# Optimization experiments

Hardware: AMD Instinct MI355X
Metric: run time of the kernel (lower is better)

The kernel has to match this reference:

```python
import jax, jax.numpy as jnp
import numpy as np

B, N, DIM, K = 4, 4096, 128, 16


def setup_inputs() -> dict:
    key = jax.random.key(0)
    ks = jax.random.split(key, 20)
    s = 0.05
    inp = {
        "x": jax.random.normal(ks[0], (B, N, DIM), jnp.float32),
        "pos": jax.random.normal(ks[1], (B, N, 3), jnp.float32),
        # pos_mlp: Linear(3,dim) -> ReLU -> Linear(dim,dim)
        "pw1": jax.random.normal(ks[2], (3, DIM), jnp.float32) * s,
        "pb1": jnp.zeros((DIM,), jnp.float32),
        "pw2": jax.random.normal(ks[3], (DIM, DIM), jnp.float32) * s,
        "pb2": jnp.zeros((DIM,), jnp.float32),
        # q/k/v projections
        "qw": jax.random.normal(ks[4], (DIM, DIM), jnp.float32) * s,
        "qb": jnp.zeros((DIM,), jnp.float32),
        "kw": jax.random.normal(ks[5], (DIM, DIM), jnp.float32) * s,
        "kb": jnp.zeros((DIM,), jnp.float32),
        "vw": jax.random.normal(ks[6], (DIM, DIM), jnp.float32) * s,
        "vb": jnp.zeros((DIM,), jnp.float32),
        # attn MLP: Linear(dim, dim//4) -> ReLU -> Linear(dim//4, dim)
        "aw1": jax.random.normal(ks[7], (DIM, DIM // 4), jnp.float32) * s,
        "ab1": jnp.zeros((DIM // 4,), jnp.float32),
        "aw2": jax.random.normal(ks[8], (DIM // 4, DIM), jnp.float32) * s,
        "ab2": jnp.zeros((DIM,), jnp.float32),
    }
    return inp


def reference(x, pos, pw1, pb1, pw2, pb2, qw, qb, kw, kb, vw, vb, aw1, ab1, aw2, ab2):
    Bs, Np, C = x.shape
    k = K
    # pairwise squared distances: |pi|^2 + |pj|^2 - 2 pi.pj  -> (B,N,N)
    inner = jnp.einsum('bnd,bmd->bnm', pos, pos)
    xx = jnp.sum(pos * pos, axis=2, keepdims=True)  # (B,N,1)
    dist = xx + jnp.swapaxes(xx, 1, 2) - 2.0 * inner
    # k nearest neighbors (smallest dist) -> indices (B,N,k)
    _, idx = jax.lax.top_k(-dist, k)
    bidx = jnp.arange(Bs)[:, None, None]
    neighbors = x[bidx, idx]        # (B,N,k,C)
    pos_neighbors = pos[bidx, idx]  # (B,N,k,3)
    pos_relative = pos[:, :, None, :] - pos_neighbors  # (B,N,k,3)
    # pos MLP
    pe = jax.nn.relu(pos_relative @ pw1 + pb1) @ pw2 + pb2  # (B,N,k,C)
    q = (x @ qw + qb)[:, :, None, :]   # (B,N,1,C)
    kk = neighbors @ kw + kb           # (B,N,k,C)
    v = neighbors @ vw + vb            # (B,N,k,C)
    a = q - kk + pe
    attn = jax.nn.relu(a @ aw1 + ab1) @ aw2 + ab2  # (B,N,k,C)
    attn = jax.nn.softmax(attn, axis=2)
    out = jnp.sum(attn * (v + pe), axis=2)  # (B,N,C)
    return out
```

## Files before the change

### kernel.cpp

```cpp
#include <hip/hip_runtime.h>
#include <hip/hip_bf16.h>
#include <stdint.h>

#define BATCH 4
#define NPTS  4096
#define DIM   128
#define KNN   16
#define NROWS (BATCH*NPTS)
#define NCHUNK 16
#define CHUNK  (NPTS/NCHUNK)

typedef unsigned long long u64;
typedef unsigned int u32;
typedef unsigned short u16;
typedef __attribute__((ext_vector_type(8))) short short8;
typedef __attribute__((ext_vector_type(4))) float f32x4;

__device__ __forceinline__ u16 f2bf(float f) {
  u32 u = __float_as_uint(f);
  u += 0x7FFFu + ((u >> 16) & 1);
  return (u16)(u >> 16);
}

__global__ __launch_bounds__(256) void prep_pos4(const float* __restrict__ pos,
                                                 float4* __restrict__ pos4) {
  int i = blockIdx.x * 256 + threadIdx.x;
  if (i < NROWS) pos4[i] = make_float4(pos[3*i], pos[3*i+1], pos[3*i+2], 0.f);
}

__global__ __launch_bounds__(256) void prep_matmul(
    const float* __restrict__ pw2, const float* __restrict__ qw, const float* __restrict__ kw,
    const float* __restrict__ aw1,
    u16* __restrict__ w1T, float* __restrict__ Wq2, float* __restrict__ Wk2) {
  int p = blockIdx.x >> 2, qtr = blockIdx.x & 3;
  const float* A = p == 0 ? pw2 : (p == 1 ? qw : kw);
  int j = threadIdx.x & 31;
  int r0 = qtr*32 + (threadIdx.x >> 5)*4;
  float acc[4] = {0.f,0.f,0.f,0.f};
  for (int c = 0; c < 128; ++c) {
    float av = aw1[c*32 + j];
#pragma unroll
    for (int rr = 0; rr < 4; ++rr) acc[rr] = fmaf(A[(r0+rr)*128 + c], av, acc[rr]);
  }
#pragma unroll
  for (int rr = 0; rr < 4; ++rr) {
    int h = r0 + rr;
    if (p == 0)      w1T[j*128 + (h ^ ((j&7)<<3))] = f2bf(acc[rr]);
    else if (p == 1) Wq2[h*32 + j] = acc[rr];
    else             Wk2[h*32 + j] = acc[rr];
  }
}

__global__ __launch_bounds__(256) void prep_convert(
    const float* __restrict__ pw2, const float* __restrict__ aw2,
    const float* __restrict__ pw1, const float* __restrict__ pb1,
    const float* __restrict__ qb, const float* __restrict__ kb,
    const float* __restrict__ pb2, const float* __restrict__ aw1, const float* __restrict__ ab1,
    u16* __restrict__ pw2T, u16* __restrict__ aw2T,
    float4* __restrict__ pw1q, float* __restrict__ bias1) {
  int bid = blockIdx.x, tid = threadIdx.x;
  if (bid < 64) {
    int e = bid*256 + tid; int k = e >> 7, n = e & 127;
    pw2T[n*128 + (k ^ ((n&7)<<3))] = f2bf(pw2[k*128 + n]);
  } else if (bid < 80) {
    int e = (bid-64)*256 + tid; int k = e >> 7, n = e & 127;
    aw2T[n*32 + (k ^ ((n&3)<<3))] = f2bf(aw2[k*128 + n]);
  } else {
    if (tid < 128) {
      int c = tid;
      pw1q[c ^ ((c & 0x18) >> 2)] = make_float4(pw1[c], pw1[128+c], pw1[256+c], pb1[c]);
    } else if (tid < 160) {
      int j = tid - 128;
      float s = ab1[j];
      for (int c = 0; c < 128; ++c) s += (qb[c]-kb[c]+pb2[c]) * aw1[c*32+j];
      bias1[j] = s;
    }
  }
}

template <typename T>
__device__ __forceinline__ void cex(T& a, T& b) {
  T mn = a < b ? a : b;
  T mx = a < b ? b : a;
  a = mn; b = mx;
}
template <typename T>
__device__ __forceinline__ void sort16(T x[16]) {
#pragma unroll
  for (int k = 2; k <= 16; k <<= 1)
#pragma unroll
    for (int j = k >> 1; j > 0; j >>= 1)
#pragma unroll
      for (int i = 0; i < 16; ++i) {
        int l = i ^ j;
        if (l > i) { if ((i & k) == 0) cex(x[i], x[l]); else cex(x[l], x[i]); }
      }
}
template <typename T>
__device__ __forceinline__ void merge16(T A[16], const T B[16]) {
#pragma unroll
  for (int i = 0; i < 16; ++i) { T b = B[15 - i]; A[i] = A[i] < b ? A[i] : b; }
#pragma unroll
  for (int j = 8; j > 0; j >>= 1)
#pragma unroll
    for (int i = 0; i < 16; ++i) { int l = i ^ j; if (l > i) cex(A[i], A[l]); }
}

__global__ __launch_bounds__(256) void knn_scan(const float4* __restrict__ pos4,
                                                u32* __restrict__ part) {
  __shared__ float4 cs[4][CHUNK];
  const int lane  = threadIdx.x & 63;
  const int w     = threadIdx.x >> 6;
  const int task  = blockIdx.x * 4 + w;
  const int qg    = task >> 4;
  const int chunk = task & 15;
  const int qbase = qg * 64;
  const int b     = qbase >> 12;
  const int cbase = chunk * CHUNK;

  const float4* cand = pos4 + b*NPTS + cbase;
#pragma unroll
  for (int i = 0; i < CHUNK/64; ++i) cs[w][lane + 64*i] = cand[lane + 64*i];
  __syncthreads();

  float4 qp = pos4[qbase + lane];
  const float qx = qp.x, qy = qp.y, qz = qp.z;

  u32 best[16];
#pragma unroll
  for (int i = 0; i < 16; ++i) best[i] = ~0u;

#pragma unroll 1
  for (int m = 0; m < CHUNK/16; ++m) {
    u32 batch[16];
#pragma unroll
    for (int e = 0; e < 16; ++e) {
      float4 p = cs[w][m*16 + e];
      float dx = qx - p.x, dy = qy - p.y, dz = qz - p.z;
      float d  = fmaf(dx, dx, fmaf(dy, dy, dz*dz));
      batch[e] = (__float_as_uint(d) & 0xFFFFFF00u) | (u32)(m*16 + e);
    }
    sort16(batch);
    merge16(best, batch);
  }
  const int q = qbase + lane;
#pragma unroll
  for (int s = 0; s < 16; ++s) part[(chunk*16 + s)*NROWS + q] = best[s];
}

__global__ __launch_bounds__(256) void knn_refine(const float4* __restrict__ pos4,
                                                  const u32* __restrict__ part,
                                                  int* __restrict__ knnIdx) {
  __shared__ u64 lists[16][273];
  const int tid = threadIdx.x;
  const int qi = tid >> 4, c = tid & 15;
  const int q = blockIdx.x * 16 + qi;
  const int b = q >> 12;

  float4 qp = pos4[q];
  const double qx = qp.x, qy = qp.y, qz = qp.z;

  u64 key[16];
#pragma unroll
  for (int s = 0; s < 16; ++s) {
    u32 kk = part[(c*16 + s)*NROWS + q];
    int idx = c*CHUNK + (int)(kk & 0xFFu);
    float4 p = pos4[(b<<12) + idx];
    double dx = qx - (double)p.x;
    double dy = qy - (double)p.y;
    double dz = qz - (double)p.z;
    double d  = fma(dx, dx, fma(dy, dy, dz*dz));
    key[s] = (((u64)__double_as_longlong(d)) & ~0xFFFull) | (u64)idx;
  }
  sort16(key);
#pragma unroll
  for (int s = 0; s < 16; ++s) lists[qi][c*17 + s] = key[s];
  __syncthreads();

  if ((tid & 15) == 0) {
    u64 best[16];
#pragma unroll
    for (int s = 0; s < 16; ++s) best[s] = lists[qi][s];
#pragma unroll 1
    for (int cc = 1; cc < 16; ++cc) {
      u64 nb[16];
#pragma unroll
      for (int s = 0; s < 16; ++s) nb[s] = lists[qi][cc*17 + s];
      merge16(best, nb);
    }
    const int outq = q * KNN;
#pragma unroll
    for (int s = 0; s < 16; ++s) knnIdx[outq + s] = (int)(best[s] & 0xFFFull);
  }
}

__global__ __launch_bounds__(256) void proj_v(
    const float* __restrict__ x,
    const float* __restrict__ vw, const float* __restrict__ vb,
    const float* __restrict__ Wq2, const float* __restrict__ Wk2,
    float* __restrict__ vo, float* __restrict__ qa, float* __restrict__ ka) {
  __shared__ float xs[32*DIM];
  const int row0 = blockIdx.x * 32;
  const int tid = threadIdx.x;
  {
    const float4* src = (const float4*)(x + row0*DIM);
    float4* dst = (float4*)xs;
#pragma unroll
    for (int i = 0; i < 4; ++i) dst[tid + 256*i] = src[tid + 256*i];
  }
  __syncthreads();
  {
    const int c = tid & 127, g2 = tid >> 7;
    float av[16];
#pragma unroll
    for (int r = 0; r < 16; ++r) av[r] = 0.f;
    for (int d4 = 0; d4 < 32; ++d4) {
      float wv[4];
#pragma unroll
      for (int t = 0; t < 4; ++t) wv[t] = vw[(d4*4+t)*DIM + c];
#pragma unroll
      for (int r = 0; r < 16; ++r) {
        float4 xv = *(const float4*)&xs[(g2*16+r)*DIM + d4*4];
        av[r] = fmaf(xv.x, wv[0], av[r]);
        av[r] = fmaf(xv.y, wv[1], av[r]);
        av[r] = fmaf(xv.z, wv[2], av[r]);
        av[r] = fmaf(xv.w, wv[3], av[r]);
      }
    }
    float bv = vb[c];
#pragma unroll
    for (int r = 0; r < 16; ++r) vo[(row0 + g2*16 + r)*DIM + c] = av[r] + bv;
  }
  {
    const int j = tid & 31, grp = tid >> 5;
    float aq[4] = {0.f,0.f,0.f,0.f}, ak[4] = {0.f,0.f,0.f,0.f};
    for (int d4 = 0; d4 < 32; ++d4) {
#pragma unroll
      for (int t = 0; t < 4; ++t) {
        int d = d4*4 + t;
        float wq = Wq2[d*32 + j], wk = Wk2[d*32 + j];
#pragma unroll
        for (int rr = 0; rr < 4; ++rr) {
          float xv = xs[(grp*4+rr)*DIM + d];
          aq[rr] = fmaf(xv, wq, aq[rr]);
          ak[rr] = fmaf(xv, wk, ak[rr]);
        }
      }
    }
#pragma unroll
    for (int rr = 0; rr < 4; ++rr) {
      qa[(row0 + grp*4 + rr)*32 + j] = aq[rr];
      ka[(row0 + grp*4 + rr)*32 + j] = ak[rr];
    }
  }
}

__global__ __launch_bounds__(256) void attn_mfma(
    const float4* __restrict__ pos4, const int* __restrict__ knnIdx,
    const float* __restrict__ vws, const float* __restrict__ qa, const float* __restrict__ ka,
    const u16* __restrict__ pw2T, const u16* __restrict__ w1T, const u16* __restrict__ aw2T,
    const float4* __restrict__ pw1q, const float* __restrict__ bias1,
    const float* __restrict__ pb2, const float* __restrict__ ab2,
    float* __restrict__ out) {
  __shared__ __align__(16) u16 pw2s[16384];
  __shared__ __align__(16) u16 w1s[4096];
  __shared__ __align__(16) u16 aw2s[4096];
  __shared__ __align__(16) float4 pw1s[128];
  __shared__ float bias1s[32];
  __shared__ float pb2s[128];
  __shared__ float ab2s[128];
  __shared__ __align__(16) u16 h2t[4][512];
  __shared__ float4 rels[4][16];
  __shared__ int ids[4][16];

  const int tid = threadIdx.x;
  {
    const uint4* s1 = (const uint4*)pw2T; uint4* d1 = (uint4*)pw2s;
#pragma unroll
    for (int i = 0; i < 8; ++i) d1[tid + 256*i] = s1[tid + 256*i];
    const uint4* s2 = (const uint4*)w1T; uint4* d2 = (uint4*)w1s;
#pragma unroll
    for (int i = 0; i < 2; ++i) d2[tid + 256*i] = s2[tid + 256*i];
    const uint4* s3 = (const uint4*)aw2T; uint4* d3 = (uint4*)aw2s;
#pragma unroll
    for (int i = 0; i < 2; ++i) d3[tid + 256*i] = s3[tid + 256*i];
    if (tid < 128) { pw1s[tid] = pw1q[tid]; pb2s[tid] = pb2[tid]; ab2s[tid] = ab2[tid]; }
    else if (tid < 160) bias1s[tid-128] = bias1[tid-128];
  }
  __syncthreads();

  const int lane = tid & 63, w = tid >> 6;
  const int c16 = lane & 15, g = lane >> 4;

  for (int it = 0; it < 4; ++it) {
    const int q = blockIdx.x*16 + w*4 + it;
    const int b = q >> 12;
    if (lane < 16) {
      int id = knnIdx[q*KNN + lane];
      ids[w][lane] = id;
      float4 pq = pos4[q], pn = pos4[(b<<12) + id];
      rels[w][lane] = make_float4(pq.x-pn.x, pq.y-pn.y, pq.z-pn.z, 0.f);
    }
    __syncthreads();

    int idr[4];
#pragma unroll
    for (int r = 0; r < 4; ++r) idr[r] = ids[w][g*4 + r];

    float qa_v[2], ka_v[2][4];
#pragma unroll
    for (int t = 0; t < 2; ++t) qa_v[t] = qa[q*32 + t*16 + c16];
#pragma unroll
    for (int r = 0; r < 4; ++r)
#pragma unroll
      for (int t = 0; t < 2; ++t) ka_v[t][r] = ka[((b<<12)+idr[r])*32 + t*16 + c16];

    float4 rl = rels[w][c16];
    short8 h1f[4];
#pragma unroll
    for (int kc = 0; kc < 4; ++kc) {
      short8 s;
#pragma unroll
      for (int j = 0; j < 8; ++j) {
        int c = kc*32 + g*8 + j;
        float4 wv = pw1s[c ^ ((c & 0x18) >> 2)];
        float h = fmaf(rl.x, wv.x, fmaf(rl.y, wv.y, fmaf(rl.z, wv.z, wv.w)));
        s[j] = (short)f2bf(fmaxf(h, 0.f));
      }
      h1f[kc] = s;
    }

    f32x4 pe[8];
#pragma unroll
    for (int nt = 0; nt < 8; ++nt) { f32x4 z = {0.f,0.f,0.f,0.f}; pe[nt] = z; }
#pragma unroll
    for (int kc = 0; kc < 4; ++kc)
#pragma unroll
      for (int nt = 0; nt < 8; ++nt) {
        int n = nt*16 + c16;
        short8 bf = *(const short8*)&pw2s[n*128 + ((kc*32 + g*8) ^ ((n&7)<<3))];
        pe[nt] = __builtin_amdgcn_mfma_f32_16x16x32_bf16(h1f[kc], bf, pe[nt], 0, 0, 0);
      }

    f32x4 ha[2];
#pragma unroll
    for (int t = 0; t < 2; ++t) { f32x4 z = {0.f,0.f,0.f,0.f}; ha[t] = z; }
#pragma unroll
    for (int kc = 0; kc < 4; ++kc)
#pragma unroll
      for (int t = 0; t < 2; ++t) {
        int n = t*16 + c16;
        short8 bf = *(const short8*)&w1s[n*128 + ((kc*32 + g*8) ^ ((n&7)<<3))];
        ha[t] = __builtin_amdgcn_mfma_f32_16x16x32_bf16(h1f[kc], bf, ha[t], 0, 0, 0);
      }

#pragma unroll
    for (int t = 0; t < 2; ++t)
#pragma unroll
      for (int r = 0; r < 4; ++r) {
        float v = ha[t][r] + qa_v[t] - ka_v[t][r] + bias1s[t*16 + c16];
        int row = g*4 + r, col = t*16 + c16;
        h2t[w][row*32 + (col ^ ((row&3)<<3))] = f2bf(fmaxf(v, 0.f));
      }
    __syncthreads();

    short8 h2f = *(const short8*)&h2t[w][c16*32 + ((g*8) ^ ((c16&3)<<3))];

    f32x4 lg[8];
#pragma unroll
    for (int nt = 0; nt < 8; ++nt) {
      int n = nt*16 + c16;
      float ab = ab2s[n];
      f32x4 cini = {ab, ab, ab, ab};
      short8 bf = *(const short8*)&aw2s[n*32 + ((g*8) ^ ((n&3)<<3))];
      lg[nt] = __builtin_amdgcn_mfma_f32_16x16x32_bf16(h2f, bf, cini, 0, 0, 0);
    }

    float vv[8][4];
#pragma unroll
    for (int r = 0; r < 4; ++r) {
      const float* vrow = vws + (size_t)((b<<12) + idr[r])*DIM;
#pragma unroll
      for (int nt = 0; nt < 8; ++nt) vv[nt][r] = vrow[nt*16 + c16];
    }

#pragma unroll
    for (int nt = 0; nt < 8; ++nt) {
      float m = fmaxf(fmaxf(lg[nt][0], lg[nt][1]), fmaxf(lg[nt][2], lg[nt][3]));
      m = fmaxf(m, __shfl_xor(m, 16));
      m = fmaxf(m, __shfl_xor(m, 32));
      float e0 = __expf(lg[nt][0]-m), e1 = __expf(lg[nt][1]-m),
            e2 = __expf(lg[nt][2]-m), e3 = __expf(lg[nt][3]-m);
      float s = e0+e1+e2+e3;
      s += __shfl_xor(s, 16);
      s += __shfl_xor(s, 32);
      float inv = 1.0f / s;
      float pb = pb2s[nt*16 + c16];
      float acc = e0*(vv[nt][0] + pe[nt][0] + pb)
                + e1*(vv[nt][1] + pe[nt][1] + pb)
                + e2*(vv[nt][2] + pe[nt][2] + pb)
                + e3*(vv[nt][3] + pe[nt][3] + pb);
      acc *= inv;
      acc += __shfl_xor(acc, 16);
      acc += __shfl_xor(acc, 32);
      if (lane < 16) out[q*DIM + nt*16 + lane] = acc;
    }
  }
}

extern "C" void kernel_launch(void* const* d_in, const int* in_sizes, int n_in,
                              void* d_out, int out_size, void* d_ws, size_t ws_size,
                              hipStream_t stream) {
  const float* x   = (const float*)d_in[0];
  const float* pos = (const float*)d_in[1];
  const float* pw1 = (const float*)d_in[2];
  const float* pb1 = (const float*)d_in[3];
  const float* pw2 = (const float*)d_in[4];
  const float* pb2 = (const float*)d_in[5];
  const float* qw  = (const float*)d_in[6];
  const float* qb  = (const float*)d_in[7];
  const float* kw  = (const float*)d_in[8];
  const float* kb  = (const float*)d_in[9];
  const float* vw  = (const float*)d_in[10];
  const float* vb  = (const float*)d_in[11];
  const float* aw1 = (const float*)d_in[12];
  const float* ab1 = (const float*)d_in[13];
  const float* aw2 = (const float*)d_in[14];
  const float* ab2 = (const float*)d_in[15];
  float* out = (float*)d_out;

  char* ws = (char*)d_ws;
  float4* pos4   = (float4*)(ws);
  int*    knnIdx = (int*)(ws + (1u<<20));
  u32*    part   = (u32*)(ws + (2u<<20));
  float*  vws    = (float*)(ws + (2u<<20));
  float*  qa     = (float*)(ws + (11u<<20));
  float*  ka     = (float*)(ws + (13u<<20));
  char*   wsw    = ws + (19u<<20);
  u16*    pw2T  = (u16*)(wsw);
  u16*    w1T   = (u16*)(wsw + 32768);
  u16*    aw2T  = (u16*)(wsw + 40960);
  float4* pw1q  = (float4*)(wsw + 49152);
  float*  bias1 = (float*)(wsw + 51200);
  float*  Wq2   = (float*)(wsw + 51328);
  float*  Wk2   = (float*)(wsw + 67712);

  prep_pos4<<<NROWS/256, 256, 0, stream>>>(pos, pos4);
  prep_matmul<<<12, 256, 0, stream>>>(pw2, qw, kw, aw1, w1T, Wq2, Wk2);
  prep_convert<<<81, 256, 0, stream>>>(pw2, aw2, pw1, pb1, qb, kb, pb2, aw1, ab1,
                                       pw2T, aw2T, pw1q, bias1);
  knn_scan<<<(NROWS/64)*NCHUNK/4, 256, 0, stream>>>(pos4, part);
  knn_refine<<<NROWS/16, 256, 0, stream>>>(pos4, part, knnIdx);
  proj_v<<<NROWS/32, 256, 0, stream>>>(x, vw, vb, Wq2, Wk2, vws, qa, ka);
  attn_mfma<<<NROWS/16, 256, 0, stream>>>(pos4, knnIdx, vws, qa, ka,
                                          pw2T, w1T, aw2T, pw1q, bias1, pb2, ab2, out);
}
```

Measured before the change: 284.2 us.

## Parallelize KNN refine with bitonic tree merge and fp64 rescoring of top-32

The scan kernel now packs a global candidate index into 12 low bits and stores each query's partial lists contiguously with vector stores. The refine kernel reads them with uint4 loads and merges the 16 chunk lists with a parallel bitonic tree in shared memory, replacing the single-thread serial merge. Only the surviving 32 candidates are rescored in double precision and then merged to the final 16, instead of rescoring all 256. The risk is that coarser fp32 keys (12 bits of mantissa dropped) may leave a true neighbour outside the top 32 in near-tie cases.

```diff
diff --git a/kernel.cpp b/kernel.cpp
--- a/kernel.cpp
+++ b/kernel.cpp
@@ -105,6 +105,12 @@
 #pragma unroll
     for (int i = 0; i < 16; ++i) { int l = i ^ j; if (l > i) cex(A[i], A[l]); }
 }
+__device__ __forceinline__ void bmerge32(u32 x[32]) {
+#pragma unroll
+  for (int j = 16; j > 0; j >>= 1)
+#pragma unroll
+    for (int i = 0; i < 32; ++i) { int l = i ^ j; if (l > i) cex(x[i], x[l]); }
+}
 
 __global__ __launch_bounds__(256) void knn_scan(const float4* __restrict__ pos4,
                                                 u32* __restrict__ part) {
@@ -138,56 +144,119 @@
       float4 p = cs[w][m*16 + e];
       float dx = qx - p.x, dy = qy - p.y, dz = qz - p.z;
       float d  = fmaf(dx, dx, fmaf(dy, dy, dz*dz));
-      batch[e] = (__float_as_uint(d) & 0xFFFFFF00u) | (u32)(m*16 + e);
+      batch[e] = (__float_as_uint(d) & 0xFFFFF000u) | (u32)(cbase + m*16 + e);
     }
     sort16(batch);
     merge16(best, batch);
   }
   const int q = qbase + lane;
-#pragma unroll
-  for (int s = 0; s < 16; ++s) part[(chunk*16 + s)*NROWS + q] = best[s];
+  uint4* dst = (uint4*)(part + q*256 + chunk*16);
+#pragma unroll
+  for (int t = 0; t < 4; ++t)
+    dst[t] = make_uint4(best[4*t], best[4*t+1], best[4*t+2], best[4*t+3]);
 }
 
 __global__ __launch_bounds__(256) void knn_refine(const float4* __restrict__ pos4,
                                                   const u32* __restrict__ part,
                                                   int* __restrict__ knnIdx) {
-  __shared__ u64 lists[16][273];
+  __shared__ u64 A64[16][137];
+  __shared__ u32 Bu[16][264];
+  u32 (*Au)[274] = (u32 (*)[274])A64;
+
   const int tid = threadIdx.x;
   const int qi = tid >> 4, c = tid & 15;
-  const int q = blockIdx.x * 16 + qi;
-  const int b = q >> 12;
-
-  float4 qp = pos4[q];
-  const double qx = qp.x, qy = qp.y, qz = qp.z;
-
-  u64 key[16];
-#pragma unroll
-  for (int s = 0; s < 16; ++s) {
-    u32 kk = part[(c*16 + s)*NROWS + q];
-    int idx = c*CHUNK + (int)(kk & 0xFFu);
-    float4 p = pos4[(b<<12) + idx];
-    double dx = qx - (double)p.x;
-    double dy = qy - (double)p.y;
-    double dz = qz - (double)p.z;
-    double d  = fma(dx, dx, fma(dy, dy, dz*dz));
-    key[s] = (((u64)__double_as_longlong(d)) & ~0xFFFull) | (u64)idx;
-  }
-  sort16(key);
-#pragma unroll
-  for (int s = 0; s < 16; ++s) lists[qi][c*17 + s] = key[s];
-  __syncthreads();
-
-  if ((tid & 15) == 0) {
-    u64 best[16];
-#pragma unroll
-    for (int s = 0; s < 16; ++s) best[s] = lists[qi][s];
-#pragma unroll 1
-    for (int cc = 1; cc < 16; ++cc) {
-      u64 nb[16];
-#pragma unroll
-      for (int s = 0; s < 16; ++s) nb[s] = lists[qi][cc*17 + s];
-      merge16(best, nb);
-    }
+  const int q  = blockIdx.x * 16 + qi;
+  const int b  = q >> 12;
+
+  {
+    const uint4* src = (const uint4*)(part + q*256 + c*16);
+    u32 own[16];
+#pragma unroll
+    for (int t = 0; t < 4; ++t) {
+      uint4 v = src[t];
+      own[4*t+0]=v.x; own[4*t+1]=v.y; own[4*t+2]=v.z; own[4*t+3]=v.w;
+    }
+#pragma unroll
+    for (int s = 0; s < 16; ++s) Au[qi][c*17 + s] = own[s];
+  }
+  __syncthreads();
+
+  if (c < 8) {
+    u32 x[32];
+#pragma unroll
+    for (int s = 0; s < 16; ++s) x[s]      = Au[qi][(2*c)*17 + s];
+#pragma unroll
+    for (int s = 0; s < 16; ++s) x[16 + s] = Au[qi][(2*c+1)*17 + 15 - s];
+    bmerge32(x);
+#pragma unroll
+    for (int s = 0; s < 32; ++s) Bu[qi][c*33 + s] = x[s];
+  }
+  __syncthreads();
+
+  if (c < 4) {
+    u32 x[32];
+#pragma unroll
+    for (int s = 0; s < 32; ++s) {
+      u32 a = Bu[qi][(2*c)*33 + s], bb = Bu[qi][(2*c+1)*33 + 31 - s];
+      x[s] = a < bb ? a : bb;
+    }
+    bmerge32(x);
+#pragma unroll
+    for (int s = 0; s < 32; ++s) Au[qi][c*33 + s] = x[s];
+  }
+  __syncthreads();
+
+  if (c < 2) {
+    u32 x[32];
+#pragma unroll
+    for (int s = 0; s < 32; ++s) {
+      u32 a = Au[qi][(2*c)*33 + s], bb = Au[qi][(2*c+1)*33 + 31 - s];
+      x[s] = a < bb ? a : bb;
+    }
+    bmerge32(x);
+#pragma unroll
+    for (int s = 0; s < 32; ++s) Bu[qi][c*33 + s] = x[s];
+  }
+  __syncthreads();
+
+  if (c == 0) {
+    u32 x[32];
+#pragma unroll
+    for (int s = 0; s < 32; ++s) {
+      u32 a = Bu[qi][s], bb = Bu[qi][33 + 31 - s];
+      x[s] = a < bb ? a : bb;
+    }
+    bmerge32(x);
+#pragma unroll
+    for (int s = 0; s < 32; ++s) Bu[qi][132 + s] = x[s];
+  }
+  __syncthreads();
+
+  if (c < 2) {
+    float4 qp = pos4[q];
+    const double qx = qp.x, qy = qp.y, qz = qp.z;
+    u64 key[16];
+#pragma unroll
+    for (int s = 0; s < 16; ++s) {
+      int idx = (int)(Bu[qi][132 + c*16 + s] & 0xFFFu);
+      float4 p = pos4[(b<<12) + idx];
+      double dx = qx - (double)p.x;
+      double dy = qy - (double)p.y;
+      double dz = qz - (double)p.z;
+      double d  = fma(dx, dx, fma(dy, dy, dz*dz));
+      key[s] = (((u64)__double_as_longlong(d)) & ~0xFFFull) | (u64)idx;
+    }
+    sort16(key);
+#pragma unroll
+    for (int s = 0; s < 16; ++s) A64[qi][c*17 + s] = key[s];
+  }
+  __syncthreads();
+
+  if (c == 0) {
+    u64 best[16], nb[16];
+#pragma unroll
+    for (int s = 0; s < 16; ++s) { best[s] = A64[qi][s]; nb[s] = A64[qi][17 + s]; }
+    merge16(best, nb);
     const int outq = q * KNN;
 #pragma unroll
     for (int s = 0; s < 16; ++s) knnIdx[outq + s] = (int)(best[s] & 0xFFFull);
```

Measured after the change: 251.8 us. 1.13x faster.
